# Kernel optimization log

Hardware: AMD Instinct MI355X
Metric: run time of the kernel (lower is better)

## Reference

```python
import jax, jax.numpy as jnp
import numpy as np

EMB = 1024
HEADS = 16
HEAD_DIM = EMB // HEADS


def setup_inputs() -> dict:
    key = jax.random.key(0)
    ks = jax.random.split(key, 5)
    B, N = 2, 2048
    x = jax.random.normal(ks[0], (B, N, EMB), dtype=jnp.float32)
    # nn.Linear(emb, 3*emb): weight [3*emb, emb], bias [3*emb]
    lim_qkv = 1.0 / np.sqrt(EMB)
    qkv_w = jax.random.uniform(ks[1], (3 * EMB, EMB), minval=-lim_qkv, maxval=lim_qkv, dtype=jnp.float32)
    qkv_b = jax.random.uniform(ks[2], (3 * EMB,), minval=-lim_qkv, maxval=lim_qkv, dtype=jnp.float32)
    proj_w = jax.random.uniform(ks[3], (EMB, EMB), minval=-lim_qkv, maxval=lim_qkv, dtype=jnp.float32)
    proj_b = jax.random.uniform(ks[4], (EMB,), minval=-lim_qkv, maxval=lim_qkv, dtype=jnp.float32)
    return {"x": x, "qkv_w": qkv_w, "qkv_b": qkv_b, "proj_w": proj_w, "proj_b": proj_b}


def reference(x, qkv_w, qkv_b, proj_w, proj_b):
    B, N, C = x.shape
    scale = HEAD_DIM ** -0.5
    # qkv: [B, N, 3*C] -> [3, B, H, N, hd]
    qkv = (jnp.einsum('bnc,dc->bnd', x, qkv_w) + qkv_b)
    qkv = qkv.reshape(B, N, 3, HEADS, HEAD_DIM).transpose(2, 0, 3, 1, 4)
    q, k, v = qkv[0], qkv[1], qkv[2]
    attn = jnp.einsum('bhqd,bhkd->bhqk', q, k) * scale  # [B,H,N,N]
    attn = jax.nn.softmax(attn, axis=-1)
    out = jnp.einsum('bhqk,bhkd->bhqd', attn, v)  # [B,H,N,hd]
    out = out.transpose(0, 2, 1, 3).reshape(B, N, C)
    return jnp.einsum('bnc,dc->bnd', out, proj_w) + proj_b
```

## Files before the change

kernel.cpp:

```cpp
#include <hip/hip_runtime.h>
#include <hip/hip_bf16.h>

typedef __hip_bfloat16 bf16;
typedef __attribute__((ext_vector_type(8))) short short8;
typedef __attribute__((ext_vector_type(4))) float f32x4;
typedef __attribute__((ext_vector_type(4))) unsigned short us4;
typedef __attribute__((ext_vector_type(4))) unsigned int u32x4;

#define EMB 1024
#define HEADS 16
#define HD 64
#define BATCH 2
#define SEQ 2048
#define ROWS (BATCH * SEQ)

#define QSCALE (0.125f * 1.44269504088896340736f)

__device__ __forceinline__ void gload_lds16(const void* g, void* l) {
  __builtin_amdgcn_global_load_lds(
      (const __attribute__((address_space(1))) void*)g,
      (__attribute__((address_space(3))) void*)l, 16, 0, 0);
}

__device__ __forceinline__ unsigned short f2bf(float x) {
  bf16 h = __float2bfloat16(x);
  return __builtin_bit_cast(unsigned short, h);
}

__device__ __forceinline__ unsigned int cvtpk(float lo, float hi) {
  unsigned int r;
  asm("v_cvt_pk_bf16_f32 %0, %1, %2" : "=v"(r) : "v"(lo), "v"(hi));
  return r;
}

__device__ __forceinline__ float fexp2(float x) {
  float r;
  asm("v_exp_f32 %0, %1" : "=v"(r) : "v"(x));
  return r;
}

__global__ __launch_bounds__(256) void cvt3_kernel(
    const float* __restrict__ a, const float* __restrict__ b,
    const float* __restrict__ cc, unsigned short* __restrict__ oa,
    unsigned short* __restrict__ ob, unsigned short* __restrict__ oc, int na4,
    int nb4, int nc4) {
  int i = blockIdx.x * 256 + threadIdx.x;
  const float* src;
  unsigned short* dst;
  int j = i;
  if (j < na4) {
    src = a;
    dst = oa;
  } else if ((j -= na4) < nb4) {
    src = b;
    dst = ob;
  } else if ((j -= nb4) < nc4) {
    src = cc;
    dst = oc;
  } else {
    return;
  }
  const float4 v = ((const float4*)src)[j];
  us4 o;
  o[0] = f2bf(v.x);
  o[1] = f2bf(v.y);
  o[2] = f2bf(v.z);
  o[3] = f2bf(v.w);
  ((us4*)dst)[j] = o;
}

template <int MODE>
__global__ __launch_bounds__(256) void gemm_bt(
    const bf16* __restrict__ A, const bf16* __restrict__ B,
    const float* __restrict__ bias,
    unsigned short* __restrict__ out0, unsigned short* __restrict__ out1,
    unsigned short* __restrict__ out2, float* __restrict__ outF, int N, int K) {
  __shared__ unsigned short As[128 * 64];
  __shared__ unsigned short Bs[128 * 64];
  const int lane = threadIdx.x & 63;
  const int wv = threadIdx.x >> 6;
  const int m0 = blockIdx.y * 128;
  const int n0 = blockIdx.x * 128;
  const int wr = wv >> 1, wc = wv & 1;

  f32x4 acc[4][4] = {};

  const int srow = lane >> 3;
  const int scol = (lane & 7) * 8;
  const bf16* Ag = A + (size_t)(m0 + wv * 32 + srow) * K + scol;
  const bf16* Bg = B + (size_t)(n0 + wv * 32 + srow) * K + scol;

  for (int k0 = 0; k0 < K; k0 += 64) {
#pragma unroll
    for (int i = 0; i < 4; ++i) {
      gload_lds16(Ag + (size_t)(i * 8) * K + k0, As + (wv * 32 + i * 8) * 64);
      gload_lds16(Bg + (size_t)(i * 8) * K + k0, Bs + (wv * 32 + i * 8) * 64);
    }
    __syncthreads();
#pragma unroll
    for (int kk = 0; kk < 2; ++kk) {
      short8 a[4], b[4];
#pragma unroll
      for (int i = 0; i < 4; ++i)
        a[i] = *(const short8*)(As + (wr * 64 + i * 16 + (lane & 15)) * 64 +
                                kk * 32 + (lane >> 4) * 8);
#pragma unroll
      for (int i = 0; i < 4; ++i)
        b[i] = *(const short8*)(Bs + (wc * 64 + i * 16 + (lane & 15)) * 64 +
                                kk * 32 + (lane >> 4) * 8);
#pragma unroll
      for (int mi = 0; mi < 4; ++mi)
#pragma unroll
        for (int ni = 0; ni < 4; ++ni)
          acc[mi][ni] = __builtin_amdgcn_mfma_f32_16x16x32_bf16(
              a[mi], b[ni], acc[mi][ni], 0, 0, 0);
    }
    __syncthreads();
  }

#pragma unroll
  for (int mi = 0; mi < 4; ++mi) {
#pragma unroll
    for (int ni = 0; ni < 4; ++ni) {
      const int col = n0 + wc * 64 + ni * 16 + (lane & 15);
      const float bv = bias[col];
#pragma unroll
      for (int r = 0; r < 4; ++r) {
        const int row = m0 + wr * 64 + mi * 16 + (lane >> 4) * 4 + r;
        float v = acc[mi][ni][r] + bv;
        if (MODE == 0) {
          const int part = col >> 10;
          const int h = (col & 1023) >> 6;
          const int hd = col & 63;
          const int bb = row >> 11;
          const int tok = row & 2047;
          const size_t bh = (size_t)(bb * HEADS + h);
          if (part == 0) {
            out0[(bh * SEQ + tok) * HD + hd] = f2bf(v * QSCALE);
          } else if (part == 1) {
            out1[(bh * SEQ + tok) * HD + hd] = f2bf(v);
          } else {
            out2[(bh * HD + hd) * SEQ + tok] = f2bf(v);
          }
        } else {
          outF[(size_t)row * N + col] = v;
        }
      }
    }
  }
}

#define STAGE(B, KV0)                                                        \
  do {                                                                       \
    _Pragma("unroll") for (int i = 0; i < 2; ++i) {                          \
      const int row = (wv << 4) + (i << 3) + (lane >> 3);                    \
      gload_lds16(Kx + base + (size_t)((KV0) + row) * HD + swz8,             \
                  (void*)&Kb[B][((wv << 4) + (i << 3)) << 6]);               \
      gload_lds16(Vt + base + (size_t)row * SEQ + (KV0) + swz8,              \
                  (void*)&Vb[B][((wv << 4) + (i << 3)) << 6]);               \
    }                                                                        \
  } while (0)

__global__ __launch_bounds__(256, 2) void attn_kernel(
    const bf16* __restrict__ Q, const bf16* __restrict__ Kx,
    const bf16* __restrict__ Vt, unsigned short* __restrict__ O) {
  __shared__ unsigned short Kb[2][64 * 64];
  __shared__ unsigned short Vb[2][64 * 64];
  const int lane = threadIdx.x & 63;
  const int wv = threadIdx.x >> 6;
  const int c = lane & 15;
  const int q4 = lane >> 4;
  const int bh = blockIdx.x;
  const int b = bh >> 4;
  const int h = bh & 15;
  const int q0 = blockIdx.y * 128 + wv * 32;
  const size_t base = (size_t)bh * SEQ * HD;
  const int swz8 = ((lane & 7) ^ (lane >> 3)) * 8;
  const int p7 = c & 7;
  const int kOff0 = (q4 ^ p7) * 8;
  const int kOff1 = ((4 + q4) ^ p7) * 8;

  const int idx0 = (((q4 & 1) << 5) | c) << 2;
  const int idx1 = idx0 + 64;
  const bool hiSel = q4 >= 2;

  short8 qf[2][2];
#pragma unroll
  for (int blk = 0; blk < 2; ++blk)
#pragma unroll
    for (int kk = 0; kk < 2; ++kk)
      qf[blk][kk] = *(const short8*)(Q + base +
                                     (size_t)(q0 + blk * 16 + c) * HD +
                                     kk * 32 + q4 * 8);

  f32x4 oT[2][4] = {};
  float l[2] = {0.f, 0.f};
  const f32x4 initC = {-4.0f, -4.0f, -4.0f, -4.0f};

  STAGE(0, 0);
  int cur = 0;
  for (int t = 0; t < SEQ / 64; ++t) {
    __syncthreads();
    if (t + 1 < SEQ / 64) STAGE(cur ^ 1, (t + 1) * 64);

    short8 kf[2][4];
#pragma unroll
    for (int n = 0; n < 4; ++n) {
      kf[0][n] = *(const short8*)&Kb[cur][(n * 16 + c) * 64 + kOff0];
      kf[1][n] = *(const short8*)&Kb[cur][(n * 16 + c) * 64 + kOff1];
    }

    f32x4 sT[2][4];
#pragma unroll
    for (int blk = 0; blk < 2; ++blk)
#pragma unroll
      for (int n = 0; n < 4; ++n) sT[blk][n] = initC;
    __builtin_amdgcn_s_setprio(1);
#pragma unroll
    for (int kk = 0; kk < 2; ++kk)
#pragma unroll
      for (int n = 0; n < 4; ++n)
#pragma unroll
        for (int blk = 0; blk < 2; ++blk)
          sT[blk][n] = __builtin_amdgcn_mfma_f32_16x16x32_bf16(
              kf[kk][n], qf[blk][kk], sT[blk][n], 0, 0, 0);
    __builtin_amdgcn_s_setprio(0);

    short8 vf[2][4];
#pragma unroll
    for (int n = 0; n < 4; ++n) {
      vf[0][n] = *(const short8*)&Vb[cur][(n * 16 + c) * 64 + kOff0];
      vf[1][n] = *(const short8*)&Vb[cur][(n * 16 + c) * 64 + kOff1];
    }

#pragma unroll
    for (int blk = 0; blk < 2; ++blk) {
      unsigned int W[4][2];
      float rs = 0.f;
#pragma unroll
      for (int n = 0; n < 4; ++n) {
        const float p0 = fexp2(sT[blk][n][0]);
        const float p1 = fexp2(sT[blk][n][1]);
        const float p2 = fexp2(sT[blk][n][2]);
        const float p3 = fexp2(sT[blk][n][3]);
        rs += (p0 + p1) + (p2 + p3);
        W[n][0] = cvtpk(p0, p1);
        W[n][1] = cvtpk(p2, p3);
      }

      __builtin_amdgcn_s_setprio(1);
#pragma unroll
      for (int kk = 0; kk < 2; ++kk) {
        u32x4 tw;
#pragma unroll
        for (int w = 0; w < 4; ++w) {
          const int idx = (w >> 1) ? idx1 : idx0;
          const int rp = w & 1;
          const int blo = __builtin_amdgcn_ds_bpermute(idx, (int)W[2 * kk][rp]);
          const int bhi =
              __builtin_amdgcn_ds_bpermute(idx, (int)W[2 * kk + 1][rp]);
          tw[w] = (unsigned int)(hiSel ? bhi : blo);
        }
        const short8 pb = __builtin_bit_cast(short8, tw);
#pragma unroll
        for (int nd = 0; nd < 4; ++nd)
          oT[blk][nd] = __builtin_amdgcn_mfma_f32_16x16x32_bf16(
              vf[kk][nd], pb, oT[blk][nd], 0, 0, 0);
      }
      __builtin_amdgcn_s_setprio(0);

      rs += __shfl_xor(rs, 16);
      rs += __shfl_xor(rs, 32);
      l[blk] += rs;
    }
    cur ^= 1;
  }

#pragma unroll
  for (int blk = 0; blk < 2; ++blk) {
    const int row = blk * 16 + c;
    const float inv = 1.0f / l[blk];
#pragma unroll
    for (int nd = 0; nd < 4; ++nd) {
      us4 ov;
      ov[0] = f2bf(oT[blk][nd][0] * inv);
      ov[1] = f2bf(oT[blk][nd][1] * inv);
      ov[2] = f2bf(oT[blk][nd][2] * inv);
      ov[3] = f2bf(oT[blk][nd][3] * inv);
      *(us4*)&O[((size_t)b * SEQ + q0 + row) * EMB + h * HD + nd * 16 +
                q4 * 4] = ov;
    }
  }
}

extern "C" void kernel_launch(void* const* d_in, const int* in_sizes, int n_in,
                              void* d_out, int out_size, void* d_ws,
                              size_t ws_size, hipStream_t stream) {
  const float* x = (const float*)d_in[0];
  const float* qkv_w = (const float*)d_in[1];
  const float* qkv_b = (const float*)d_in[2];
  const float* proj_w = (const float*)d_in[3];
  const float* proj_b = (const float*)d_in[4];

  const size_t n_x = (size_t)ROWS * EMB;
  const size_t n_qkvw = (size_t)3 * EMB * EMB;
  const size_t n_projw = (size_t)EMB * EMB;
  const size_t elems = (size_t)BATCH * HEADS * SEQ * HD;

  unsigned short* xb = (unsigned short*)d_ws;
  unsigned short* wqkv = xb + n_x;
  unsigned short* wproj = wqkv + n_qkvw;
  unsigned short* Qw = wproj + n_projw;
  unsigned short* Kw = Qw + elems;
  unsigned short* Vw = Kw + elems;
  unsigned short* Ow = Vw + elems;

  const int na4 = (int)(n_x / 4), nb4 = (int)(n_qkvw / 4),
            nc4 = (int)(n_projw / 4);
  cvt3_kernel<<<(na4 + nb4 + nc4 + 255) / 256, 256, 0, stream>>>(
      x, qkv_w, proj_w, xb, wqkv, wproj, na4, nb4, nc4);

  dim3 g1(3 * EMB / 128, ROWS / 128);
  gemm_bt<0><<<g1, 256, 0, stream>>>((const bf16*)xb, (const bf16*)wqkv, qkv_b,
                                     Qw, Kw, Vw, nullptr, 3 * EMB, EMB);

  dim3 g2(BATCH * HEADS, SEQ / 128);
  attn_kernel<<<g2, 256, 0, stream>>>((const bf16*)Qw, (const bf16*)Kw,
                                      (const bf16*)Vw, Ow);

  dim3 g3(EMB / 128, ROWS / 128);
  gemm_bt<1><<<g3, 256, 0, stream>>>((const bf16*)Ow, (const bf16*)wproj,
                                     proj_b, nullptr, nullptr, nullptr,
                                     (float*)d_out, EMB, EMB);
}
```

Before: 160.0 us.

## Double-buffer GEMM LDS tiles with prefetch and XOR-swizzle shared layout

The bf16 GEMM now keeps two LDS buffers per operand and issues the next K-tile's global-to-LDS loads right after the barrier, overlapping them with MFMA work on the current tile and dropping one barrier per iteration. Global load columns and LDS reads are XOR-swizzled by row so that the 16-byte fragment reads spread across banks. The LDS footprint doubles to 64KB per block, which can lower occupancy.

```diff
diff --git a/kernel.cpp b/kernel.cpp
--- a/kernel.cpp
+++ b/kernel.cpp
@@ -69,14 +69,24 @@
   ((us4*)dst)[j] = o;
 }
 
+#define GSTAGE(BUF, KOFF)                                                 \
+  do {                                                                    \
+    _Pragma("unroll") for (int i = 0; i < 4; ++i) {                       \
+      gload_lds16(Ag + (size_t)(i * 8) * K + (KOFF),                      \
+                  (void*)&As[BUF][(wv * 32 + i * 8) * 64]);               \
+      gload_lds16(Bg + (size_t)(i * 8) * K + (KOFF),                      \
+                  (void*)&Bs[BUF][(wv * 32 + i * 8) * 64]);               \
+    }                                                                     \
+  } while (0)
+
 template <int MODE>
 __global__ __launch_bounds__(256) void gemm_bt(
     const bf16* __restrict__ A, const bf16* __restrict__ B,
     const float* __restrict__ bias,
     unsigned short* __restrict__ out0, unsigned short* __restrict__ out1,
     unsigned short* __restrict__ out2, float* __restrict__ outF, int N, int K) {
-  __shared__ unsigned short As[128 * 64];
-  __shared__ unsigned short Bs[128 * 64];
+  __shared__ unsigned short As[2][128 * 64];
+  __shared__ unsigned short Bs[2][128 * 64];
   const int lane = threadIdx.x & 63;
   const int wv = threadIdx.x >> 6;
   const int m0 = blockIdx.y * 128;
@@ -86,28 +96,29 @@
   f32x4 acc[4][4] = {};
 
   const int srow = lane >> 3;
-  const int scol = (lane & 7) * 8;
-  const bf16* Ag = A + (size_t)(m0 + wv * 32 + srow) * K + scol;
-  const bf16* Bg = B + (size_t)(n0 + wv * 32 + srow) * K + scol;
-
+  const int sswz = (((lane & 7) ^ srow) & 7) * 8;
+  const bf16* Ag = A + (size_t)(m0 + wv * 32 + srow) * K + sswz;
+  const bf16* Bg = B + (size_t)(n0 + wv * 32 + srow) * K + sswz;
+
+  const int c = lane & 15;
+  const int q4 = lane >> 4;
+  const int rx = c & 7;
+
+  GSTAGE(0, 0);
+  int cur = 0;
   for (int k0 = 0; k0 < K; k0 += 64) {
-#pragma unroll
-    for (int i = 0; i < 4; ++i) {
-      gload_lds16(Ag + (size_t)(i * 8) * K + k0, As + (wv * 32 + i * 8) * 64);
-      gload_lds16(Bg + (size_t)(i * 8) * K + k0, Bs + (wv * 32 + i * 8) * 64);
-    }
     __syncthreads();
+    if (k0 + 64 < K) GSTAGE(cur ^ 1, k0 + 64);
 #pragma unroll
     for (int kk = 0; kk < 2; ++kk) {
+      const int chunk = ((kk * 4 + q4) ^ rx) * 8;
       short8 a[4], b[4];
 #pragma unroll
       for (int i = 0; i < 4; ++i)
-        a[i] = *(const short8*)(As + (wr * 64 + i * 16 + (lane & 15)) * 64 +
-                                kk * 32 + (lane >> 4) * 8);
+        a[i] = *(const short8*)&As[cur][(wr * 64 + i * 16 + c) * 64 + chunk];
 #pragma unroll
       for (int i = 0; i < 4; ++i)
-        b[i] = *(const short8*)(Bs + (wc * 64 + i * 16 + (lane & 15)) * 64 +
-                                kk * 32 + (lane >> 4) * 8);
+        b[i] = *(const short8*)&Bs[cur][(wc * 64 + i * 16 + c) * 64 + chunk];
 #pragma unroll
       for (int mi = 0; mi < 4; ++mi)
 #pragma unroll
@@ -115,18 +126,18 @@
           acc[mi][ni] = __builtin_amdgcn_mfma_f32_16x16x32_bf16(
               a[mi], b[ni], acc[mi][ni], 0, 0, 0);
     }
-    __syncthreads();
+    cur ^= 1;
   }
 
 #pragma unroll
   for (int mi = 0; mi < 4; ++mi) {
 #pragma unroll
     for (int ni = 0; ni < 4; ++ni) {
-      const int col = n0 + wc * 64 + ni * 16 + (lane & 15);
+      const int col = n0 + wc * 64 + ni * 16 + c;
       const float bv = bias[col];
 #pragma unroll
       for (int r = 0; r < 4; ++r) {
-        const int row = m0 + wr * 64 + mi * 16 + (lane >> 4) * 4 + r;
+        const int row = m0 + wr * 64 + mi * 16 + q4 * 4 + r;
         float v = acc[mi][ni][r] + bv;
         if (MODE == 0) {
           const int part = col >> 10;
```

Result: faster. 144.7 us (-9.6%).
